# Kernel optimization log

Measured on AMD Instinct MI355X. Metric: run time of the kernel, lower is better.

Reference implementation:

```python
import jax, jax.numpy as jnp
import numpy as np

HEADS = 16
DIM_HEAD = 64
LN_EPS = 1e-5
COS_EPS = 1e-8


def setup_inputs() -> dict:
    key = jax.random.key(0)
    ks = jax.random.split(key, 5)
    dim = 1024
    inner = HEADS * DIM_HEAD
    q = jax.random.normal(ks[0], (4, 1024, dim), dtype=jnp.float32)
    k = jax.random.normal(ks[1], (4, 2048, dim), dtype=jnp.float32)
    v = jax.random.normal(ks[2], (4, 2048, dim), dtype=jnp.float32)
    W_in = jax.random.normal(ks[3], (dim, inner), dtype=jnp.float32) * (1.0 / np.sqrt(dim))
    W_out = jax.random.normal(ks[4], (inner, dim), dtype=jnp.float32) * (1.0 / np.sqrt(inner))
    ln_gamma = jnp.ones((dim,), dtype=jnp.float32)
    ln_beta = jnp.zeros((dim,), dtype=jnp.float32)
    b_out = jnp.zeros((dim,), dtype=jnp.float32)
    return {"q": q, "k": k, "v": v, "ln_gamma": ln_gamma, "ln_beta": ln_beta,
            "W_in": W_in, "W_out": W_out, "b_out": b_out}


def _layernorm(x, gamma, beta):
    mu = jnp.mean(x, axis=-1, keepdims=True)
    var = jnp.mean(jnp.square(x - mu), axis=-1, keepdims=True)  # biased, as torch
    return (x - mu) * jax.lax.rsqrt(var + LN_EPS) * gamma + beta


def _project(t, gamma, beta, W_in):
    # LayerNorm -> Linear(no bias) -> split heads: b n (h d) -> b h n d
    x = _layernorm(t, gamma, beta) @ W_in
    b, n, _ = x.shape
    return x.reshape(b, n, HEADS, DIM_HEAD).transpose(0, 2, 1, 3)


def reference(q, k, v, ln_gamma, ln_beta, W_in, W_out, b_out):
    f_q = _project(q, ln_gamma, ln_beta, W_in)  # [b,h,n,d]
    f_k = _project(k, ln_gamma, ln_beta, W_in)  # [b,h,m,d]
    f_v = _project(v, ln_gamma, ln_beta, W_in)  # [b,h,m,d]
    dots = jnp.einsum('bhnd,bhmd->bhnm', f_q, f_k)
    qn = jnp.linalg.norm(f_q, axis=-1, keepdims=True)          # [b,h,n,1]
    kn = jnp.linalg.norm(f_k, axis=-1, keepdims=True)          # [b,h,m,1]
    attn = dots / (qn * kn.transpose(0, 1, 3, 2) + COS_EPS)    # [b,h,n,m]
    out = jnp.einsum('bhnm,bhmd->bhnd', attn, f_v)             # [b,h,n,d]
    b, h, n, d = out.shape
    out = out.transpose(0, 2, 1, 3).reshape(b, n, h * d)       # b n (h d)
    return out @ W_out + b_out
```

## Files before the change

kernel.cpp:

```cpp
#include <hip/hip_runtime.h>

constexpr int BATCH = 4;
constexpr int SEQQ  = 1024;
constexpr int SEQK  = 2048;
constexpr int DIM   = 1024;
constexpr int NH    = 16;
constexpr int DH    = 64;
constexpr int RQ    = BATCH * SEQQ;
constexpr int RK    = BATCH * SEQK;
constexpr int RTOT  = RQ + 2 * RK;
constexpr int BH    = BATCH * NH;
constexpr int NSLC  = 8;
constexpr float LN_EPS = 1e-5f;

typedef _Float16 f16;
typedef __attribute__((ext_vector_type(8))) _Float16 f16x8;
typedef __attribute__((ext_vector_type(4))) float f32x4;

__device__ __forceinline__ void async16(const void* g, void* l) {
  __builtin_amdgcn_global_load_lds(
      (const __attribute__((address_space(1))) void*)g,
      (__attribute__((address_space(3))) void*)l, 16, 0, 0);
}

__global__ void __launch_bounds__(256) ln_to_f16(
    const float* __restrict__ q, const float* __restrict__ k,
    const float* __restrict__ v, const float* __restrict__ gamma,
    const float* __restrict__ beta, f16* __restrict__ a_h) {
  const int row = blockIdx.x * 4 + (threadIdx.x >> 6);
  const int lane = threadIdx.x & 63;
  const float* src;
  if (row < RQ)            src = q + (size_t)row * DIM;
  else if (row < RQ + RK)  src = k + (size_t)(row - RQ) * DIM;
  else                     src = v + (size_t)(row - RQ - RK) * DIM;
  float4 x[4];
  float s = 0.f, s2 = 0.f;
#pragma unroll
  for (int c = 0; c < 4; c++) {
    x[c] = ((const float4*)src)[c * 64 + lane];
    s  += x[c].x + x[c].y + x[c].z + x[c].w;
    s2 += x[c].x * x[c].x + x[c].y * x[c].y + x[c].z * x[c].z + x[c].w * x[c].w;
  }
#pragma unroll
  for (int off = 1; off < 64; off <<= 1) {
    s  += __shfl_xor(s, off);
    s2 += __shfl_xor(s2, off);
  }
  const float mu = s / DIM;
  const float rs = rsqrtf(s2 / DIM - mu * mu + LN_EPS);
#pragma unroll
  for (int c = 0; c < 4; c++) {
    float4 g = ((const float4*)gamma)[c * 64 + lane];
    float4 b = ((const float4*)beta)[c * 64 + lane];
    union { f16 h[4]; uint2 u; } o;
    o.h[0] = (f16)((x[c].x - mu) * rs * g.x + b.x);
    o.h[1] = (f16)((x[c].y - mu) * rs * g.y + b.y);
    o.h[2] = (f16)((x[c].z - mu) * rs * g.z + b.z);
    o.h[3] = (f16)((x[c].w - mu) * rs * g.w + b.w);
    ((uint2*)(a_h + (size_t)row * DIM))[c * 64 + lane] = o.u;
  }
}

__global__ void __launch_bounds__(256) transpose_f16(
    const float* __restrict__ W0, const float* __restrict__ W1,
    f16* __restrict__ T0, f16* __restrict__ T1) {
  const float* W = blockIdx.z ? W1 : W0;
  f16* T = blockIdx.z ? T1 : T0;
  __shared__ float tile[32][33];
  int tx = threadIdx.x & 31, ty = threadIdx.x >> 5;
  int k0 = blockIdx.x * 32, n0 = blockIdx.y * 32;
#pragma unroll
  for (int i = 0; i < 4; i++)
    tile[ty + 8 * i][tx] = W[(size_t)(k0 + ty + 8 * i) * DIM + n0 + tx];
  __syncthreads();
#pragma unroll
  for (int i = 0; i < 4; i++)
    T[(size_t)(n0 + ty + 8 * i) * DIM + k0 + tx] = (f16)tile[tx][ty + 8 * i];
}

constexpr int PT_A = 320 * 64;
constexpr int PT_B = 256 * 64;

#define STAGE_A(buf, kt) do {                                        \
    const f16* s_ = gA + (size_t)(kt) * 64;                          \
    f16* d_ = AsW + (buf) * PT_A;                                    \
    async16(s_,          d_);                                        \
    async16(s_ +  65536, d_ + 4096);                                 \
    async16(s_ + 131072, d_ + 8192);                                 \
    async16(s_ + 196608, d_ + 12288);                                \
    async16(s_ + 262144, d_ + 16384);                                \
  } while (0)

#define STAGE_B(buf, kt) do {                                        \
    const f16* s_ = gB + (size_t)(kt) * 64;                          \
    f16* d_ = BsW + (buf) * PT_B;                                    \
    async16(s_,          d_);                                        \
    async16(s_ +  65536, d_ + 4096);                                 \
    async16(s_ + 131072, d_ + 8192);                                 \
    async16(s_ + 196608, d_ + 12288);                                \
  } while (0)

#define WT5 asm volatile("s_waitcnt vmcnt(5)" ::: "memory")
#define WT0 asm volatile("s_waitcnt vmcnt(0)" ::: "memory")
#define WTN ((void)0)
#define STN ((void)0)

#define PH(BUF, H, MH, RB, STG, WT) {                                \
    STG;                                                             \
    __builtin_amdgcn_sched_barrier(0);                               \
    WT;                                                              \
    __builtin_amdgcn_s_barrier();                                    \
    __builtin_amdgcn_sched_barrier(0);                               \
    if (RB) {                                                        \
      _Pragma("unroll") for (int j_ = 0; j_ < 4; ++j_)               \
        bf[j_] = *(const f16x8*)(bB##H + (BUF) * PT_B + j_ * 1024);  \
    }                                                                \
    _Pragma("unroll") for (int f_ = 0; f_ < 5; ++f_)                 \
      af[f_] = *(const f16x8*)(aB##H + (BUF) * PT_A + (MH) * 5120 +  \
                               f_ * 1024);                           \
    __builtin_amdgcn_s_setprio(1);                                   \
    _Pragma("unroll") for (int f_ = 0; f_ < 5; ++f_)                 \
      _Pragma("unroll") for (int j_ = 0; j_ < 4; ++j_)               \
        acc[(MH) * 5 + f_][j_] = __builtin_amdgcn_mfma_f32_16x16x32_f16( \
            af[f_], bf[j_], acc[(MH) * 5 + f_][j_], 0, 0, 0);        \
    __builtin_amdgcn_s_setprio(0);                                   \
    __builtin_amdgcn_sched_barrier(0);                               \
    __builtin_amdgcn_s_barrier();                                    \
  }

__global__ void __launch_bounds__(512, 2) proj_gemm(
    const f16* __restrict__ A, const f16* __restrict__ Bt,
    f16* __restrict__ C) {
  __shared__ __align__(16) f16 As[2 * PT_A];
  __shared__ __align__(16) f16 Bs[2 * PT_B];

  const int tid = threadIdx.x;
  const int wid = tid >> 6;
  const int lane = tid & 63;
  const int la15 = lane & 15;

  const int bid = blockIdx.x;
  const int swz = (bid & 7) * 32 + (bid >> 3);
  const int row0 = (swz >> 2) * 320;
  const int col0 = (swz & 3) * 256;

  const int wm = (wid >> 2) * 160;
  const int wn = (wid & 3) * 64;

  const int hs = (tid & 7) ^ ((tid >> 3) & 7);
  const f16* gA = A + (size_t)(row0 + (tid >> 3)) * DIM + (hs >> 2) * 32 +
                  (hs & 3) * 8;
  const f16* gB = Bt + (size_t)(col0 + (tid >> 3)) * DIM + (hs >> 2) * 32 +
                  (hs & 3) * 8;
  f16* AsW = As + wid * 512;
  f16* BsW = Bs + wid * 512;

  const int g = lane >> 4;
  const int r7 = la15 & 7;
  const int cs0 = (g ^ r7) * 8;
  const int cs1 = ((4 + g) ^ r7) * 8;
  const f16* aB0 = As + (wm + la15) * 64 + cs0;
  const f16* aB1 = As + (wm + la15) * 64 + cs1;
  const f16* bB0 = Bs + (wn + la15) * 64 + cs0;
  const f16* bB1 = Bs + (wn + la15) * 64 + cs1;

  f32x4 acc[10][4];
#pragma unroll
  for (int i = 0; i < 10; i++)
#pragma unroll
    for (int j = 0; j < 4; j++) acc[i][j] = (f32x4){0.f, 0.f, 0.f, 0.f};
  f16x8 af[5], bf[4];

  STAGE_A(0, 0);
  STAGE_B(0, 0);
  __builtin_amdgcn_sched_barrier(0);
  WT0;
  __builtin_amdgcn_s_barrier();
  __builtin_amdgcn_sched_barrier(0);

#pragma unroll 1
  for (int it = 0; it < 7; ++it) {
    const int t1 = 2 * it + 1, t2 = 2 * it + 2;
    PH(0, 0, 0, 1, STAGE_A(1, t1), WT5)
    PH(0, 0, 1, 0, STAGE_B(1, t1), WTN)
    PH(0, 1, 0, 1, STN,            WTN)
    PH(0, 1, 1, 0, STN,            WTN)
    PH(1, 0, 0, 1, STAGE_A(0, t2), WT5)
    PH(1, 0, 1, 0, STAGE_B(0, t2), WTN)
    PH(1, 1, 0, 1, STN,            WTN)
    PH(1, 1, 1, 0, STN,            WTN)
  }
  PH(0, 0, 0, 1, STAGE_A(1, 15), WT5)
  PH(0, 0, 1, 0, STAGE_B(1, 15), WTN)
  PH(0, 1, 0, 1, STN,            WTN)
  PH(0, 1, 1, 0, STN,            WTN)
  PH(1, 0, 0, 1, STN,            WT0)
  PH(1, 0, 1, 0, STN,            WTN)
  PH(1, 1, 0, 1, STN,            WTN)
  PH(1, 1, 1, 0, STN,            WTN)

  const int crow = (lane >> 4) * 4;
#pragma unroll
  for (int mh = 0; mh < 2; ++mh)
#pragma unroll
    for (int f = 0; f < 5; ++f) {
      const int m = mh * 5 + f;
      const int rbase = row0 + wm + mh * 80 + f * 16 + crow;
#pragma unroll
      for (int r = 0; r < 4; ++r) {
        float s = acc[m][0][r] * acc[m][0][r] + acc[m][1][r] * acc[m][1][r]
                + acc[m][2][r] * acc[m][2][r] + acc[m][3][r] * acc[m][3][r];
        s += __shfl_xor(s, 1);
        s += __shfl_xor(s, 2);
        s += __shfl_xor(s, 4);
        s += __shfl_xor(s, 8);
        if (rbase + r < RQ + RK) {
          const float inv = rsqrtf(s);
#pragma unroll
          for (int j = 0; j < 4; ++j) acc[m][j][r] *= inv;
        }
      }
    }

#pragma unroll
  for (int j = 0; j < 4; ++j) {
    const int col = col0 + wn + j * 16 + la15;
#pragma unroll
    for (int m = 0; m < 10; ++m) {
      const int rb = row0 + wm + (m / 5) * 80 + (m % 5) * 16 + crow;
      f16* Cp = C + (size_t)rb * DIM + col;
#pragma unroll
      for (int r = 0; r < 4; ++r) Cp[(size_t)r * DIM] = (f16)acc[m][j][r];
    }
  }
}

template <int MT, bool OUT_F16, bool NORMS, bool BIAS, bool PERB>
__global__ void __launch_bounds__(256) mfma_gemm(
    const f16* __restrict__ A, const f16* __restrict__ Bt,
    void* __restrict__ Cout, const float* __restrict__ bias) {
  constexpr int JT = (MT == 128) ? 4 : 2;
  __shared__ f16 Asl[2][MT * 32];
  __shared__ f16 Bsl[2][128 * 32];
  const int t = threadIdx.x;
  const int wid = t >> 6;
  const int lane = t & 63;
  const int row0 = blockIdx.x * MT;
  const int col0 = blockIdx.y * 128;
  const int wm = (MT == 128) ? (wid >> 1) * 64 : 0;
  const int wn = (MT == 128) ? (wid & 1) * 64 : wid * 32;

  const f16* BtB = PERB ? Bt + (size_t)(row0 >> 10) * DIM * DIM : Bt;

  const int rB = 32 * wid + (lane >> 2);
  const int qB = ((lane & 3) - ((rB >> 1) & 3)) & 3;
  const f16* gB = BtB + (size_t)(col0 + rB) * DIM + qB * 8;
  f16* lB0 = Bsl[0] + 32 * wid * 32;
  f16* lB1 = Bsl[1] + 32 * wid * 32;
  const int rA = (MT == 128 ? 32 : 16) * wid + (lane >> 2);
  const int qA = ((lane & 3) - ((rA >> 1) & 3)) & 3;
  const f16* gA = A + (size_t)(row0 + rA) * DIM + qA * 8;
  f16* lA0 = Asl[0] + (MT == 128 ? 32 : 16) * wid * 32;
  f16* lA1 = Asl[1] + (MT == 128 ? 32 : 16) * wid * 32;

  f32x4 acc[4][JT];
#pragma unroll
  for (int i = 0; i < 4; i++)
#pragma unroll
    for (int j = 0; j < JT; j++) acc[i][j] = (f32x4){0.f, 0.f, 0.f, 0.f};

  const int mrow = lane & 15;
  const int kq_p = (((lane >> 4) + ((lane >> 1) & 3)) & 3) * 8;

  for (int kt = 0; kt < DIM / 64; ++kt) {
    if (kt) __syncthreads();
    const int ko = kt * 64;
    async16(gA + ko,      lA0);
    if (MT == 128) async16(gA + ko + 16 * DIM, lA0 + 512);
    async16(gB + ko,      lB0);
    async16(gB + ko + 16 * DIM, lB0 + 512);
    async16(gA + ko + 32, lA1);
    if (MT == 128) async16(gA + ko + 32 + 16 * DIM, lA1 + 512);
    async16(gB + ko + 32, lB1);
    async16(gB + ko + 32 + 16 * DIM, lB1 + 512);
    __syncthreads();

#pragma unroll
    for (int h = 0; h < 2; ++h) {
      f16x8 af[4], bf[JT];
#pragma unroll
      for (int i = 0; i < 4; i++)
        af[i] = *(const f16x8*)(Asl[h] + (wm + i * 16 + mrow) * 32 + kq_p);
#pragma unroll
      for (int j = 0; j < JT; j++)
        bf[j] = *(const f16x8*)(Bsl[h] + (wn + j * 16 + mrow) * 32 + kq_p);
#pragma unroll
      for (int i = 0; i < 4; i++)
#pragma unroll
        for (int j = 0; j < JT; j++)
          acc[i][j] = __builtin_amdgcn_mfma_f32_16x16x32_f16(af[i], bf[j], acc[i][j], 0, 0, 0);
    }
  }

  if (NORMS && MT == 128) {
    if (row0 < RQ + RK) {
      float sums[4][4];
#pragma unroll
      for (int i = 0; i < 4; i++)
#pragma unroll
        for (int r = 0; r < 4; r++) {
          float s = 0.f;
#pragma unroll
          for (int j = 0; j < JT; j++) s += acc[i][j][r] * acc[i][j][r];
          sums[i][r] = s;
        }
#pragma unroll
      for (int off = 1; off < 16; off <<= 1)
#pragma unroll
        for (int i = 0; i < 4; i++)
#pragma unroll
          for (int r = 0; r < 4; r++)
            sums[i][r] += __shfl_xor(sums[i][r], off);
#pragma unroll
      for (int i = 0; i < 4; i++)
#pragma unroll
        for (int r = 0; r < 4; r++) {
          const float inv = rsqrtf(sums[i][r]);
#pragma unroll
          for (int j = 0; j < JT; j++) acc[i][j][r] *= inv;
        }
    }
  }

  const int ccol = lane & 15;
  const int crow = (lane >> 4) * 4;
  if (OUT_F16) {
    f16* C = (f16*)Cout;
#pragma unroll
    for (int j = 0; j < JT; j++) {
      const int col = col0 + wn + j * 16 + ccol;
#pragma unroll
      for (int i = 0; i < 4; i++) {
        f16* Cp = C + (size_t)(row0 + wm + i * 16 + crow) * DIM + col;
#pragma unroll
        for (int r = 0; r < 4; r++) Cp[(size_t)r * DIM] = (f16)acc[i][j][r];
      }
    }
  } else {
    float* C = (float*)Cout;
#pragma unroll
    for (int j = 0; j < JT; j++) {
      const int col = col0 + wn + j * 16 + ccol;
      float bv = BIAS ? bias[col] : 0.f;
#pragma unroll
      for (int i = 0; i < 4; i++) {
        float* Cp = C + (size_t)(row0 + wm + i * 16 + crow) * DIM + col;
#pragma unroll
        for (int r = 0; r < 4; r++) Cp[(size_t)r * DIM] = acc[i][j][r] + bv;
      }
    }
  }
}

__global__ void __launch_bounds__(256) s_kernel(
    const f16* __restrict__ f, float* __restrict__ S4) {
  const int bh = blockIdx.x;
  const int b = bh >> 4, h = bh & 15;
  const int mbase = blockIdx.y * (SEQK / NSLC);
  const int t = threadIdx.x;
  __shared__ float ks[32][68];
  __shared__ float vs[32][68];
  const int lm   = t >> 3;
  const int lseg = (t & 7) * 8;
  const int d1 = (t & 15) * 4;
  const int d2 = (t >> 4) * 4;
  float acc[4][4] = {{0.f}};
  const f16* fk_base = f + ((size_t)RQ + (size_t)b * SEQK) * DIM + h * DH;
  const f16* fv_base = f + ((size_t)RQ + RK + (size_t)b * SEQK) * DIM + h * DH;

  int m = mbase + lm;
  f16x8 kv = *(const f16x8*)(fk_base + (size_t)m * DIM + lseg);
  f16x8 vv = *(const f16x8*)(fv_base + (size_t)m * DIM + lseg);

  constexpr int SUBS = SEQK / NSLC / 32;
  for (int sub = 0; sub < SUBS; ++sub) {
    __syncthreads();
#pragma unroll
    for (int e = 0; e < 8; e++) {
      ks[lm][lseg + e] = (float)kv[e];
      vs[lm][lseg + e] = (float)vv[e];
    }
    __syncthreads();
    if (sub + 1 < SUBS) {
      m = mbase + (sub + 1) * 32 + lm;
      kv = *(const f16x8*)(fk_base + (size_t)m * DIM + lseg);
      vv = *(const f16x8*)(fv_base + (size_t)m * DIM + lseg);
    }
#pragma unroll
    for (int mm = 0; mm < 32; ++mm) {
      float4 kk = *(const float4*)&ks[mm][d1];
      float4 vv2 = *(const float4*)&vs[mm][d2];
      acc[0][0] = fmaf(kk.x, vv2.x, acc[0][0]);
      acc[0][1] = fmaf(kk.x, vv2.y, acc[0][1]);
      acc[0][2] = fmaf(kk.x, vv2.z, acc[0][2]);
      acc[0][3] = fmaf(kk.x, vv2.w, acc[0][3]);
      acc[1][0] = fmaf(kk.y, vv2.x, acc[1][0]);
      acc[1][1] = fmaf(kk.y, vv2.y, acc[1][1]);
      acc[1][2] = fmaf(kk.y, vv2.z, acc[1][2]);
      acc[1][3] = fmaf(kk.y, vv2.w, acc[1][3]);
      acc[2][0] = fmaf(kk.z, vv2.x, acc[2][0]);
      acc[2][1] = fmaf(kk.z, vv2.y, acc[2][1]);
      acc[2][2] = fmaf(kk.z, vv2.z, acc[2][2]);
      acc[2][3] = fmaf(kk.z, vv2.w, acc[2][3]);
      acc[3][0] = fmaf(kk.w, vv2.x, acc[3][0]);
      acc[3][1] = fmaf(kk.w, vv2.y, acc[3][1]);
      acc[3][2] = fmaf(kk.w, vv2.z, acc[3][2]);
      acc[3][3] = fmaf(kk.w, vv2.w, acc[3][3]);
    }
  }
  float* Sp = S4 + ((size_t)blockIdx.y * BH + bh) * DH * DH;
#pragma unroll
  for (int i = 0; i < 4; i++)
#pragma unroll
    for (int j = 0; j < 4; j++)
      Sp[(d1 + i) * DH + (d2 + j)] = acc[i][j];
}

__global__ void __launch_bounds__(256) s_reduce(
    const float* __restrict__ S4, f16* __restrict__ Sh) {
  const int bh = blockIdx.x;
  const int t = threadIdx.x;
  const size_t base = (size_t)bh * DH * DH + t * 16;
  constexpr size_t STR = (size_t)BH * DH * DH;
#pragma unroll
  for (int c = 0; c < 4; c++) {
    float4 s = {0.f, 0.f, 0.f, 0.f};
#pragma unroll
    for (int p = 0; p < NSLC; p++) {
      float4 sp = *(const float4*)(S4 + base + p * STR + 4 * c);
      s.x += sp.x; s.y += sp.y; s.z += sp.z; s.w += sp.w;
    }
    union { f16 h[4]; uint2 u; } o;
    o.h[0] = (f16)s.x; o.h[1] = (f16)s.y; o.h[2] = (f16)s.z; o.h[3] = (f16)s.w;
    *(uint2*)(Sh + base + 4 * c) = o.u;
  }
}

__global__ void __launch_bounds__(256) m_build(
    const f16* __restrict__ wt_out, const f16* __restrict__ Sh,
    f16* __restrict__ Mt) {
  const int n0 = blockIdx.x * 128;
  const int bh = blockIdx.y;
  const int b = bh >> 4, h = bh & 15;
  __shared__ f16 Asl[128 * 64];
  __shared__ f16 Bsl[64 * 64];
  const int t = threadIdx.x;
  const int wid = t >> 6, lane = t & 63;

  const f16* gA = wt_out + (size_t)(n0 + 32 * wid + (lane >> 3)) * DIM
                  + 64 * h + (lane & 7) * 8;
  f16* lA = Asl + 32 * wid * 64;
  const f16* gB = Sh + (size_t)bh * DH * DH + (16 * wid + (lane >> 3)) * 64
                  + (lane & 7) * 8;
  f16* lB = Bsl + 16 * wid * 64;
#pragma unroll
  for (int o = 0; o < 4; o++) async16(gA + (size_t)(8 * o) * DIM, lA + 8 * o * 64);
  async16(gB, lB);
  async16(gB + 8 * 64, lB + 8 * 64);
  __syncthreads();

  const int wm = (wid >> 1) * 64;
  const int wn = (wid & 1) * 32;
  const int mrow = lane & 15;
  f32x4 acc[4][2];
#pragma unroll
  for (int i = 0; i < 4; i++)
#pragma unroll
    for (int j = 0; j < 2; j++) acc[i][j] = (f32x4){0.f, 0.f, 0.f, 0.f};

#pragma unroll
  for (int kh = 0; kh < 2; kh++) {
    const int kq = kh * 32 + (lane >> 4) * 8;
    f16x8 af[4], bf[2];
#pragma unroll
    for (int i = 0; i < 4; i++)
      af[i] = *(const f16x8*)(Asl + (wm + i * 16 + mrow) * 64 + kq);
#pragma unroll
    for (int j = 0; j < 2; j++)
      bf[j] = *(const f16x8*)(Bsl + (wn + j * 16 + mrow) * 64 + kq);
#pragma unroll
    for (int i = 0; i < 4; i++)
#pragma unroll
      for (int j = 0; j < 2; j++)
        acc[i][j] = __builtin_amdgcn_mfma_f32_16x16x32_f16(af[i], bf[j], acc[i][j], 0, 0, 0);
  }

  const int ccol = lane & 15;
  const int crow = (lane >> 4) * 4;
  f16* Mb = Mt + (size_t)b * DIM * DIM;
#pragma unroll
  for (int j = 0; j < 2; j++) {
    const int col = 64 * h + wn + j * 16 + ccol;
#pragma unroll
    for (int i = 0; i < 4; i++) {
      f16* Mp = Mb + (size_t)(n0 + wm + i * 16 + crow) * DIM + col;
#pragma unroll
      for (int r = 0; r < 4; r++) Mp[(size_t)r * DIM] = (f16)acc[i][j][r];
    }
  }
}

extern "C" void kernel_launch(void* const* d_in, const int* in_sizes, int n_in,
                              void* d_out, int out_size, void* d_ws, size_t ws_size,
                              hipStream_t stream) {
  const float* q     = (const float*)d_in[0];
  const float* k     = (const float*)d_in[1];
  const float* v     = (const float*)d_in[2];
  const float* gamma = (const float*)d_in[3];
  const float* beta  = (const float*)d_in[4];
  const float* W_in  = (const float*)d_in[5];
  const float* W_out = (const float*)d_in[6];
  const float* b_out = (const float*)d_in[7];
  float* out = (float*)d_out;

  char* w = (char*)d_ws;
  f16*   f      = (f16*)w;
  f16*   a_h    = f + (size_t)RTOT * DIM;
  f16*   wt_in  = a_h + (size_t)RTOT * DIM;
  f16*   wt_out = wt_in + (size_t)DIM * DIM;
  f16*   Mt     = wt_out + (size_t)DIM * DIM;
  f16*   Sh     = Mt + (size_t)BATCH * DIM * DIM;
  float* S4     = (float*)(Sh + (size_t)BH * DH * DH);

  ln_to_f16<<<RTOT / 4, 256, 0, stream>>>(q, k, v, gamma, beta, a_h);
  transpose_f16<<<dim3(DIM / 32, DIM / 32, 2), 256, 0, stream>>>(
      W_in, W_out, wt_in, wt_out);

  proj_gemm<<<dim3(256), 512, 0, stream>>>(a_h, wt_in, f);

  s_kernel<<<dim3(BH, NSLC), 256, 0, stream>>>(f, S4);

  s_reduce<<<BH, 256, 0, stream>>>(S4, Sh);

  m_build<<<dim3(DIM / 128, BH), 256, 0, stream>>>(wt_out, Sh, Mt);

  mfma_gemm<64, false, false, true, true>
      <<<dim3(RQ / 64, DIM / 128), 256, 0, stream>>>(f, Mt, out, b_out);
}
```

Baseline: 238.9 us.

## Merge projection GEMM phases and stage output through LDS for vectorized stores

Each pipeline phase now loads the B fragments once and both A halves, then issues all 40 MFMAs, instead of splitting the work into two half-phases that each pay a barrier pair. This halves the barrier count but holds more live fragment registers. The epilogue writes accumulators into shared memory, then reads them back so each thread emits 16-byte contiguous global stores, replacing scattered 2-byte per-element stores. This adds ten extra __syncthreads rounds and reuses the As buffer as scratch.

```diff
diff --git a/kernel.cpp b/kernel.cpp
--- a/kernel.cpp
+++ b/kernel.cpp
@@ -105,24 +105,28 @@
 #define WTN ((void)0)
 #define STN ((void)0)
 
-#define PH(BUF, H, MH, RB, STG, WT) {                                \
+#define PH2(BUF, H, STG, WT) {                                       \
     STG;                                                             \
     __builtin_amdgcn_sched_barrier(0);                               \
     WT;                                                              \
     __builtin_amdgcn_s_barrier();                                    \
     __builtin_amdgcn_sched_barrier(0);                               \
-    if (RB) {                                                        \
-      _Pragma("unroll") for (int j_ = 0; j_ < 4; ++j_)               \
-        bf[j_] = *(const f16x8*)(bB##H + (BUF) * PT_B + j_ * 1024);  \
-    }                                                                \
+    _Pragma("unroll") for (int j_ = 0; j_ < 4; ++j_)                 \
+      bf[j_] = *(const f16x8*)(bB##H + (BUF) * PT_B + j_ * 1024);    \
     _Pragma("unroll") for (int f_ = 0; f_ < 5; ++f_)                 \
-      af[f_] = *(const f16x8*)(aB##H + (BUF) * PT_A + (MH) * 5120 +  \
-                               f_ * 1024);                           \
+      af0[f_] = *(const f16x8*)(aB##H + (BUF) * PT_A + f_ * 1024);   \
+    _Pragma("unroll") for (int f_ = 0; f_ < 5; ++f_)                 \
+      af1[f_] = *(const f16x8*)(aB##H + (BUF) * PT_A + 5120 +        \
+                                f_ * 1024);                          \
     __builtin_amdgcn_s_setprio(1);                                   \
     _Pragma("unroll") for (int f_ = 0; f_ < 5; ++f_)                 \
       _Pragma("unroll") for (int j_ = 0; j_ < 4; ++j_)               \
-        acc[(MH) * 5 + f_][j_] = __builtin_amdgcn_mfma_f32_16x16x32_f16( \
-            af[f_], bf[j_], acc[(MH) * 5 + f_][j_], 0, 0, 0);        \
+        acc[f_][j_] = __builtin_amdgcn_mfma_f32_16x16x32_f16(        \
+            af0[f_], bf[j_], acc[f_][j_], 0, 0, 0);                  \
+    _Pragma("unroll") for (int f_ = 0; f_ < 5; ++f_)                 \
+      _Pragma("unroll") for (int j_ = 0; j_ < 4; ++j_)               \
+        acc[5 + f_][j_] = __builtin_amdgcn_mfma_f32_16x16x32_f16(    \
+            af1[f_], bf[j_], acc[5 + f_][j_], 0, 0, 0);              \
     __builtin_amdgcn_s_setprio(0);                                   \
     __builtin_amdgcn_sched_barrier(0);                               \
     __builtin_amdgcn_s_barrier();                                    \
@@ -169,7 +173,7 @@
   for (int i = 0; i < 10; i++)
 #pragma unroll
     for (int j = 0; j < 4; j++) acc[i][j] = (f32x4){0.f, 0.f, 0.f, 0.f};
-  f16x8 af[5], bf[4];
+  f16x8 af0[5], af1[5], bf[4];
 
   STAGE_A(0, 0);
   STAGE_B(0, 0);
@@ -181,23 +185,15 @@
 #pragma unroll 1
   for (int it = 0; it < 7; ++it) {
     const int t1 = 2 * it + 1, t2 = 2 * it + 2;
-    PH(0, 0, 0, 1, STAGE_A(1, t1), WT5)
-    PH(0, 0, 1, 0, STAGE_B(1, t1), WTN)
-    PH(0, 1, 0, 1, STN,            WTN)
-    PH(0, 1, 1, 0, STN,            WTN)
-    PH(1, 0, 0, 1, STAGE_A(0, t2), WT5)
-    PH(1, 0, 1, 0, STAGE_B(0, t2), WTN)
-    PH(1, 1, 0, 1, STN,            WTN)
-    PH(1, 1, 1, 0, STN,            WTN)
-  }
-  PH(0, 0, 0, 1, STAGE_A(1, 15), WT5)
-  PH(0, 0, 1, 0, STAGE_B(1, 15), WTN)
-  PH(0, 1, 0, 1, STN,            WTN)
-  PH(0, 1, 1, 0, STN,            WTN)
-  PH(1, 0, 0, 1, STN,            WT0)
-  PH(1, 0, 1, 0, STN,            WTN)
-  PH(1, 1, 0, 1, STN,            WTN)
-  PH(1, 1, 1, 0, STN,            WTN)
+    PH2(0, 0, STAGE_A(1, t1), WT5)
+    PH2(0, 1, STAGE_B(1, t1), WTN)
+    PH2(1, 0, STAGE_A(0, t2), WT5)
+    PH2(1, 1, STAGE_B(0, t2), WTN)
+  }
+  PH2(0, 0, STAGE_A(1, 15), WT5)
+  PH2(0, 1, STAGE_B(1, 15), WTN)
+  PH2(1, 0, STN,            WT0)
+  PH2(1, 1, STN,            WTN)
 
   const int crow = (lane >> 4) * 4;
 #pragma unroll
@@ -222,17 +218,32 @@
       }
     }
 
-#pragma unroll
-  for (int j = 0; j < 4; ++j) {
-    const int col = col0 + wn + j * 16 + la15;
-#pragma unroll
-    for (int m = 0; m < 10; ++m) {
-      const int rb = row0 + wm + (m / 5) * 80 + (m % 5) * 16 + crow;
-      f16* Cp = C + (size_t)rb * DIM + col;
-#pragma unroll
-      for (int r = 0; r < 4; ++r) Cp[(size_t)r * DIM] = (f16)acc[m][j][r];
-    }
-  }
+  f16* sc = As;
+  const int wmi = wid >> 2;
+  const int ehalf = tid >> 8;
+  const int err = (tid >> 4) & 15;
+  const int ecc = tid & 15;
+  const f16* rb_l = sc + ehalf * (16 * 264) + err * 264 + ecc * 16;
+#pragma unroll
+  for (int mh = 0; mh < 2; ++mh)
+#pragma unroll
+    for (int f = 0; f < 5; ++f) {
+      const int m = mh * 5 + f;
+#pragma unroll
+      for (int j = 0; j < 4; ++j)
+#pragma unroll
+        for (int r = 0; r < 4; ++r)
+          sc[wmi * (16 * 264) + (crow + r) * 264 + wn + j * 16 + la15] =
+              (f16)acc[m][j][r];
+      __syncthreads();
+      f16x8 v0 = *(const f16x8*)(rb_l);
+      f16x8 v1 = *(const f16x8*)(rb_l + 8);
+      const int grow = row0 + ehalf * 160 + mh * 80 + f * 16 + err;
+      f16* Cp = C + (size_t)grow * DIM + col0 + ecc * 16;
+      *(f16x8*)(Cp) = v0;
+      *(f16x8*)(Cp + 8) = v1;
+      if (!(mh == 1 && f == 4)) __syncthreads();
+    }
 }
 
 template <int MT, bool OUT_F16, bool NORMS, bool BIAS, bool PERB>
```

After: 232.9 us. 2.5% less time.
